# Performance work log

Hardware: AMD Instinct MI355X
Metric: run time of the kernel (lower is better)

Reference implementation:

```python
import jax, jax.numpy as jnp
import numpy as np

# dims forced by module structure (see shape_source)
DA, DV, DD, NL, L, R0 = 128, 96, 64, 8, 2, 1.0
ATOMS, EDGES, BATCH = 5000, 40000, 1


def radial_encode_8(rvec, r0):
    # reconstruction: 8 Gaussian RBFs on |r|/r0 with centers k/7
    r = jnp.sqrt(jnp.sum(rvec * rvec, axis=-1) + 1e-12)
    u = r / r0
    k = jnp.arange(NL, dtype=u.dtype)
    return jnp.exp(-0.5 * (u[..., None] * 7.0 - k) ** 2)  # (E, 8)


def tens_sigmoid(x):
    # equivariant sigmoid: rescale vector by bounded function of its norm
    n = jnp.sqrt(jnp.sum(x * x, axis=-1, keepdims=True) + 1e-12)
    return x * (2.0 * jax.nn.sigmoid(n) - 1.0) / n


def _forward(src, dst, r_ij, x_a, x_v, x_d,
             P_000, P_110, P_220, P_011, P_101, P_121, P_211, P_111,
             P_022, P_202, P_112, P_222, P_212,
             W_in_a, W_in_v, W_in_d, W_out_a, W_out_v, W_out_d,
             Wd_a, W1_a, b1_a, W2_a, b2_a, W3_a, b3_a,
             Vd_v, V1_v, V2_v, V3_v):
    b, A = x_a.shape[:2]
    # read-in, then fuse L into the batch dim (high-actv layout)
    a = jnp.einsum('oc,bnc->bno', W_in_a, x_a).reshape(b, A, L, DA).transpose(2, 0, 1, 3).reshape(L * b, A, DA)
    v = jnp.einsum('oc,bnci->bnoi', W_in_v, x_v).reshape(b, A, L, DV, 3).transpose(2, 0, 1, 3, 4).reshape(L * b, A, DV, 3)
    d = jnp.einsum('oc,bncij->bnoij', W_in_d, x_d).reshape(b, A, L, DD, 3, 3).transpose(2, 0, 1, 3, 4, 5).reshape(L * b, A, DD, 3, 3)

    rad = radial_encode_8(r_ij, R0)              # (E, 8)
    rh = tens_sigmoid(r_ij * (7.0 / R0))         # (E, 3)
    pa = rad                                      # (E, 8)
    pv = rad[:, :, None] * rh[:, None, :]         # (E, 8, 3)
    pd = rad[:, :, None, None] * rh[:, None, None, :] * rh[:, None, :, None]  # (E, 8, 3, 3)

    # edge gather (dst nodes)
    aj, vj, dj = a[:, dst], v[:, dst], d[:, dst]

    # Ant16: 13 fused equivariant tensor-product contractions
    psi_a = (jnp.einsum('alc,el,bec->bea', P_000, pa, aj)
             + jnp.einsum('alc,eli,beci->bea', P_110, pv, vj)
             + jnp.einsum('alc,elij,becij->bea', P_220, pd, dj))

    def cross1(P, phi, xv):
        t = lambda j, k: jnp.einsum('vlc,el,bec->bev', P, phi[:, :, j], xv[:, :, :, k])
        return jnp.stack([t(1, 2) - t(2, 1), t(2, 0) - t(0, 2), t(0, 1) - t(1, 0)], axis=-1)

    psi_v = (jnp.einsum('vlc,el,beci->bevi', P_011, pa, vj)
             + jnp.einsum('vlc,eli,bec->bevi', P_101, pv, aj)
             + jnp.einsum('vlc,elj,becij->bevi', P_121, pv, dj)
             + jnp.einsum('vlc,elij,becj->bevi', P_211, pd, vj)
             + cross1(P_111, pv, vj))

    def cross2(P, phid, xv):
        t = lambda k, m: jnp.einsum('dlc,elj,bec->bedj', P, phid[:, :, k, :], xv[:, :, :, m])
        return jnp.stack([t(1, 2) - t(2, 1), t(2, 0) - t(0, 2), t(0, 1) - t(1, 0)], axis=-2)

    psi_d = (jnp.einsum('dlc,el,becij->bedij', P_022, pa, dj)
             + jnp.einsum('dlc,elij,bec->bedij', P_202, pd, aj)
             + jnp.einsum('dlc,eli,becj->bedij', P_112, pv, vj)
             + jnp.einsum('dlc,elik,beckj->bedij', P_222, pd, dj)
             + cross2(P_212, pd, vj))

    # psi_a = psi_a + MLP(psi_a);  MLP(x) = x W_d^T + 3-layer leaky-relu net
    h = jax.nn.leaky_relu(psi_a @ W1_a.T + b1_a, 0.1)
    h = jax.nn.leaky_relu(h @ W2_a.T + b2_a, 0.1)
    psi_a = psi_a + psi_a @ Wd_a.T + h @ W3_a.T + b3_a

    # psi_v = psi_v + VectorMLP(psi_v) (channel linear + tens_sigmoid, equivariant)
    hv = tens_sigmoid(jnp.einsum('oc,beci->beoi', V1_v, psi_v))
    hv = tens_sigmoid(jnp.einsum('oc,beci->beoi', V2_v, hv))
    psi_v = psi_v + jnp.einsum('oc,beci->beoi', Vd_v, psi_v) + jnp.einsum('oc,beci->beoi', V3_v, hv)

    # scatter-reduce messages onto src nodes
    Ba = jnp.zeros_like(a).at[:, src].add(psi_a)
    Bv = jnp.zeros_like(v).at[:, src].add(psi_v)
    Bd = jnp.zeros_like(d).at[:, src].add(psi_d)

    # unfuse L back into the channel dim (low-actv layout), then read out
    Ba = Ba.reshape(L, b, A, DA).transpose(1, 2, 0, 3).reshape(b, A, L * DA)
    Bv = Bv.reshape(L, b, A, DV, 3).transpose(1, 2, 0, 3, 4).reshape(b, A, L * DV, 3)
    Bd = Bd.reshape(L, b, A, DD, 3, 3).transpose(1, 2, 0, 3, 4, 5).reshape(b, A, L * DD, 3, 3)
    return (jnp.einsum('oc,bnc->bno', W_out_a, Ba),
            jnp.einsum('oc,bnci->bnoi', W_out_v, Bv),
            jnp.einsum('oc,bncij->bnoij', W_out_d, Bd))


def setup_inputs() -> dict:
    key = jax.random.key(0)
    ks = iter(jax.random.split(key, 48))
    nrm = lambda *s: jax.random.normal(next(ks), s, dtype=jnp.float32)
    nfac = (NL * max(DA, DV, DD)) ** -0.5
    P = lambda do, di: nrm(do, NL, di) * nfac
    lin = lambda do, di: nrm(do, di) * (di ** -0.5)
    return dict(
        src=jax.random.randint(next(ks), (EDGES,), 0, ATOMS),
        dst=jax.random.randint(next(ks), (EDGES,), 0, ATOMS),
        r_ij=nrm(EDGES, 3),
        x_a=nrm(BATCH, ATOMS, DA), x_v=nrm(BATCH, ATOMS, DV, 3), x_d=nrm(BATCH, ATOMS, DD, 3, 3),
        P_000=P(DA, DA), P_110=P(DA, DV), P_220=P(DA, DD),
        P_011=P(DV, DV), P_101=P(DV, DA), P_121=P(DV, DD), P_211=P(DV, DV), P_111=P(DV, DV),
        P_022=P(DD, DD), P_202=P(DD, DA), P_112=P(DD, DV), P_222=P(DD, DD), P_212=P(DD, DV),
        W_in_a=lin(DA * L, DA), W_in_v=lin(DV * L, DV), W_in_d=lin(DD * L, DD),
        W_out_a=lin(DA, DA * L), W_out_v=lin(DV, DV * L), W_out_d=lin(DD, DD * L),
        Wd_a=lin(DA, DA), W1_a=lin(2 * DA, DA), b1_a=jnp.zeros(2 * DA, jnp.float32),
        W2_a=lin(2 * DA, 2 * DA), b2_a=jnp.zeros(2 * DA, jnp.float32),
        W3_a=lin(DA, 2 * DA), b3_a=jnp.zeros(DA, jnp.float32),
        Vd_v=lin(DV, DV), V1_v=lin(2 * DV, DV), V2_v=lin(2 * DV, 2 * DV), V3_v=lin(DV, 2 * DV),
    )


def reference(src, dst, r_ij, x_a, x_v, x_d,
              P_000, P_110, P_220, P_011, P_101, P_121, P_211, P_111,
              P_022, P_202, P_112, P_222, P_212,
              W_in_a, W_in_v, W_in_d, W_out_a, W_out_v, W_out_d,
              Wd_a, W1_a, b1_a, W2_a, b2_a, W3_a, b3_a,
              Vd_v, V1_v, V2_v, V3_v):
    return _forward(src, dst, r_ij, x_a, x_v, x_d,
                    P_000, P_110, P_220, P_011, P_101, P_121, P_211, P_111,
                    P_022, P_202, P_112, P_222, P_212,
                    W_in_a, W_in_v, W_in_d, W_out_a, W_out_v, W_out_d,
                    Wd_a, W1_a, b1_a, W2_a, b2_a, W3_a, b3_a,
                    Vd_v, V1_v, V2_v, V3_v)
```

## Files before the change

### kernel.cpp

```cpp
#include <hip/hip_runtime.h>
#include <hip/hip_bf16.h>

#define NA 5000
#define NE 40000

static const int POFF[13] = {0, 131072, 229376, 294912, 368640, 466944, 516096,
                             589824, 663552, 696320, 761856, 811008, 843776};
#define A_OFF    892928
#define V_OFF    2172928
#define D_OFF    5052928
#define PHI_OFF  10812928
#define PSIA_OFF 11292928
#define PSIV_OFF 16412928
#define PSID_OFF 27932928
#define INT_OFF  50972928
#define ICNT  0
#define ICUR  5000
#define SCNT  10000
#define SCUR  15000
#define IOFF  20000
#define SOFF  25008
#define IEIDX 30016
#define ISLOT 70016
#define SPERM 110016

#define OUT_V 640000
#define OUT_D 2080000

#define WT1 0
#define WT2 32768
#define WT3 98304
#define WTD 131072
#define VT1 147456
#define VT2 165888
#define VT3 202752
#define VTD 221184

#define OFF_000 POFF[0]
#define OFF_110 POFF[1]
#define OFF_220 POFF[2]
#define OFF_011 POFF[3]
#define OFF_101 POFF[4]
#define OFF_121 POFF[5]
#define OFF_211 POFF[6]
#define OFF_111 POFF[7]
#define OFF_022 POFF[8]
#define OFF_202 POFF[9]
#define OFF_112 POFF[10]
#define OFF_222 POFF[11]
#define OFF_212 POFF[12]

__device__ __forceinline__ float dot4f(float4 a, float4 b) {
  return a.x*b.x + a.y*b.y + a.z*b.z + a.w*b.w;
}
__device__ __forceinline__ float lrelu(float x) { return x > 0.f ? x : 0.1f*x; }
__device__ __forceinline__ float bf2f(unsigned short u) {
  union { unsigned int i; float f; } x; x.i = ((unsigned int)u) << 16; return x.f;
}
__device__ __forceinline__ unsigned short f2bf(float f) {
  union { unsigned int i; float f; } x; x.f = f;
  unsigned int r = x.i + 0x7FFFu + ((x.i >> 16) & 1u);
  return (unsigned short)(r >> 16);
}

struct P13 { const float* p[13]; };
struct P8  { const float* p[8]; };

__global__ __launch_bounds__(256) void transP_all_kernel(P13 ps, float* __restrict__ Pt)
{
  static const int Od[13] = {128,128,128, 96, 96, 96, 96, 96, 64, 64, 64, 64, 64};
  static const int Cd[13] = {128, 96, 64, 96,128, 64, 96, 96, 64,128, 96, 64, 96};
  static const int POF[13] = {0, 131072, 229376, 294912, 368640, 466944, 516096,
                              589824, 663552, 696320, 761856, 811008, 843776};
  static const int CUM[14] = {0,16384,28672,36864,46080,58368,64512,73728,
                              82944,87040,95232,101376,105472,111616};
  int idx = blockIdx.x * 256 + threadIdx.x;
  if (idx >= 111616) return;
  int i = 0;
  while (idx >= CUM[i+1]) ++i;
  const int r = idx - CUM[i];
  const int O = Od[i], C = Cd[i];
  const int o = r / C, c = r % C;
  const float* src = ps.p[i];
  float* dst = Pt + POF[i];
#pragma unroll
  for (int k = 0; k < 8; ++k)
    dst[((size_t)c * O + o) * 8 + k] = src[((size_t)o * 8 + k) * C + c];
}

__global__ __launch_bounds__(256) void transW_all_kernel(P8 ps, float* __restrict__ ot)
{
  static const int R[8]   = {256,256,128,128,192,192, 96, 96};
  static const int C[8]   = {128,256,256,128, 96,192,192, 96};
  static const int CUM[9] = {0,32768,98304,131072,147456,165888,202752,221184,230400};
  int idx = blockIdx.x * 256 + threadIdx.x;
  if (idx >= 230400) return;
  int i = 0;
  while (idx >= CUM[i+1]) ++i;
  const int r = idx - CUM[i];
  const int rr = r / C[i], cc = r % C[i];
  ot[(size_t)CUM[i] + (size_t)cc * R[i] + rr] = ps.p[i][r];
}

__global__ __launch_bounds__(256) void hist2_kernel(
    const int* __restrict__ dstk, const int* __restrict__ srck,
    int* __restrict__ cntd, int* __restrict__ cnts)
{
  int e = blockIdx.x * 256 + threadIdx.x;
  if (e < NE) { atomicAdd(&cntd[dstk[e]], 1); atomicAdd(&cnts[srck[e]], 1); }
}

__global__ __launch_bounds__(256) void scan2_kernel(
    const int* __restrict__ cnt0, int* __restrict__ off0,
    const int* __restrict__ cnt1, int* __restrict__ off1)
{
  const int* cnt = (blockIdx.x == 0) ? cnt0 : cnt1;
  int* off       = (blockIdx.x == 0) ? off0 : off1;
  __shared__ int part[256];
  const int t = threadIdx.x;
  int loc[20]; int s = 0;
#pragma unroll
  for (int i = 0; i < 20; ++i) {
    int idx = t * 20 + i;
    int v = (idx < NA) ? cnt[idx] : 0;
    loc[i] = v; s += v;
  }
  part[t] = s; __syncthreads();
  for (int ofs = 1; ofs < 256; ofs <<= 1) {
    int v = (t >= ofs) ? part[t - ofs] : 0;
    __syncthreads();
    part[t] += v;
    __syncthreads();
  }
  int run = part[t] - s;
#pragma unroll
  for (int i = 0; i < 20; ++i) {
    int idx = t * 20 + i;
    if (idx < NA) off[idx] = run;
    run += loc[i];
  }
  if (t == 255) off[NA] = run;
}

__global__ __launch_bounds__(256) void sort_scatter_kernel(
    const int* __restrict__ dst, const int* __restrict__ off,
    int* __restrict__ cur, int* __restrict__ eidx, int* __restrict__ islot)
{
  int e = blockIdx.x * 256 + threadIdx.x;
  if (e >= NE) return;
  int d = dst[e];
  int pos = off[d] + atomicAdd(&cur[d], 1);
  eidx[pos] = e;
  islot[e] = pos;
}

__global__ __launch_bounds__(256) void ssort_phi_kernel(
    const int* __restrict__ src, const int* __restrict__ islot,
    const int* __restrict__ soff, int* __restrict__ scur, int* __restrict__ sperm,
    const int* __restrict__ eidx, const float* __restrict__ r_ij, float* __restrict__ phi)
{
  const int B = (NE + 255) / 256;
  if ((int)blockIdx.x < B) {
    int e = blockIdx.x * 256 + threadIdx.x;
    if (e >= NE) return;
    int s = src[e];
    int pos = soff[s] + atomicAdd(&scur[s], 1);
    sperm[pos] = islot[e];
  } else {
    int p = (blockIdx.x - B) * 256 + threadIdx.x;
    if (p >= NE) return;
    int e = eidx[p];
    const float rx = r_ij[e*3+0], ry = r_ij[e*3+1], rz = r_ij[e*3+2];
    const float r2 = rx*rx + ry*ry + rz*rz;
    const float r = sqrtf(r2 + 1e-12f);
#pragma unroll
    for (int k = 0; k < 8; ++k) {
      const float z = 7.f*r - (float)k;
      phi[(size_t)p*12 + k] = expf(-0.5f*z*z);
    }
    const float nn = sqrtf(49.f*r2 + 1e-12f);
    const float sc = (2.f / (1.f + expf(-nn)) - 1.f) / nn;
    phi[(size_t)p*12 + 8]  = 7.f*rx*sc;
    phi[(size_t)p*12 + 9]  = 7.f*ry*sc;
    phi[(size_t)p*12 + 10] = 7.f*rz*sc;
    phi[(size_t)p*12 + 11] = 0.f;
  }
}

__global__ __launch_bounds__(256) void proj_in_kernel(
    const float* __restrict__ x_a, const float* __restrict__ x_v, const float* __restrict__ x_d,
    const float* __restrict__ Wa, const float* __restrict__ Wv, const float* __restrict__ Wd,
    float* __restrict__ a_ws, float* __restrict__ v_ws, float* __restrict__ d_ws)
{
  __shared__ float xs[992];
  const int n = blockIdx.x, t = threadIdx.x;
  for (int q = t; q < 128; q += 256) xs[q]       = x_a[(size_t)n*128 + q];
  for (int q = t; q < 288; q += 256) xs[128 + q] = x_v[(size_t)n*288 + q];
  for (int q = t; q < 576; q += 256) xs[416 + q] = x_d[(size_t)n*576 + q];
  __syncthreads();
  {
    const float* W = &Wa[(size_t)t * 128];
    float acc = 0.f;
    for (int c = 0; c < 128; c += 4) acc += dot4f(*(const float4*)&W[c], *(const float4*)&xs[c]);
    int l = t >> 7, o = t & 127;
    a_ws[((size_t)l*NA + n)*128 + o] = acc;
  }
  if (t < 192) {
    const float* W = &Wv[(size_t)t * 96];
    float a0 = 0.f, a1 = 0.f, a2 = 0.f;
    for (int c = 0; c < 96; ++c) {
      float w = W[c]; const float* x = &xs[128 + c*3];
      a0 = fmaf(w, x[0], a0); a1 = fmaf(w, x[1], a1); a2 = fmaf(w, x[2], a2);
    }
    int l = t / 96, o = t % 96;
    float* dstp = &v_ws[(((size_t)l*NA + n)*96 + o)*3];
    dstp[0] = a0; dstp[1] = a1; dstp[2] = a2;
  }
  if (t < 128) {
    const float* W = &Wd[(size_t)t * 64];
    float acc[9] = {0,0,0,0,0,0,0,0,0};
    for (int c = 0; c < 64; ++c) {
      float w = W[c]; const float* x = &xs[416 + c*9];
#pragma unroll
      for (int j = 0; j < 9; ++j) acc[j] = fmaf(w, x[j], acc[j]);
    }
    int l = t >> 6, o = t & 63;
    float* dstp = &d_ws[(((size_t)l*NA + n)*64 + o)*9];
#pragma unroll
    for (int j = 0; j < 9; ++j) dstp[j] = acc[j];
  }
}

template<int O, int C, int NMU>
__device__ __forceinline__ void zcompute(const float* __restrict__ Pt,
    const float* __restrict__ xl, int o, float z[8][NMU])
{
#pragma unroll
  for (int k = 0; k < 8; ++k)
#pragma unroll
    for (int m = 0; m < NMU; ++m) z[k][m] = 0.f;
  const float* p = Pt + o * 8;
#pragma unroll 2
  for (int c = 0; c < C; ++c, p += O*8) {
    const float4 pa = *(const float4*)p;
    const float4 pb = *(const float4*)(p + 4);
#pragma unroll
    for (int m = 0; m < NMU; ++m) {
      const float xv = xl[c * NMU + m];
      z[0][m] = fmaf(pa.x, xv, z[0][m]);
      z[1][m] = fmaf(pa.y, xv, z[1][m]);
      z[2][m] = fmaf(pa.z, xv, z[2][m]);
      z[3][m] = fmaf(pa.w, xv, z[3][m]);
      z[4][m] = fmaf(pb.x, xv, z[4][m]);
      z[5][m] = fmaf(pb.y, xv, z[5][m]);
      z[6][m] = fmaf(pb.z, xv, z[6][m]);
      z[7][m] = fmaf(pb.w, xv, z[7][m]);
    }
  }
}

template<int O, int C>
__device__ __forceinline__ void zcompute_k4(const float* __restrict__ Pt,
    const float* __restrict__ xl, int o, int kh, float z[4][9])
{
#pragma unroll
  for (int k = 0; k < 4; ++k)
#pragma unroll
    for (int m = 0; m < 9; ++m) z[k][m] = 0.f;
  const float* p = Pt + o * 8 + kh * 4;
#pragma unroll 2
  for (int c = 0; c < C; ++c, p += O*8) {
    const float4 pa = *(const float4*)p;
#pragma unroll
    for (int m = 0; m < 9; ++m) {
      const float xv = xl[c*9 + m];
      z[0][m] = fmaf(pa.x, xv, z[0][m]);
      z[1][m] = fmaf(pa.y, xv, z[1][m]);
      z[2][m] = fmaf(pa.z, xv, z[2][m]);
      z[3][m] = fmaf(pa.w, xv, z[3][m]);
    }
  }
}

template<int NMU>
__device__ __forceinline__ float kdot(const float z[8][NMU], int m, const float* rr) {
  float s = z[0][m] * rr[0];
#pragma unroll
  for (int k = 1; k < 8; ++k) s = fmaf(z[k][m], rr[k], s);
  return s;
}
__device__ __forceinline__ float kdot_k4(const float z[4][9], int m, const float* rr) {
  float s = z[0][m] * rr[0];
#pragma unroll
  for (int k = 1; k < 4; ++k) s = fmaf(z[k][m], rr[k], s);
  return s;
}

#define F1_XA 0
#define F1_XV 256
#define F1_XD 832
#define F1_TOT 1984

template<int NT>
__device__ __forceinline__ void load_features1(float* sm, int t, int n,
    const float* __restrict__ a_ws, const float* __restrict__ v_ws, const float* __restrict__ d_ws)
{
  for (int q = t; q < 256; q += NT)
    sm[F1_XA + q] = a_ws[((size_t)(q>>7)*NA + n)*128 + (q & 127)];
  for (int q = t; q < 576; q += NT)
    sm[F1_XV + q] = v_ws[((size_t)(q/288)*NA + n)*288 + (q % 288)];
  for (int q = t; q < 1152; q += NT)
    sm[F1_XD + q] = d_ws[((size_t)(q/576)*NA + n)*576 + (q % 576)];
}

__global__ __launch_bounds__(256, 3) void pass_fused_kernel(
    const int* __restrict__ off, const float* __restrict__ phi,
    const float* __restrict__ Pt,
    const float* __restrict__ a_ws, const float* __restrict__ v_ws, const float* __restrict__ d_ws,
    unsigned short* __restrict__ psiA, unsigned short* __restrict__ psiV,
    unsigned short* __restrict__ psiD)
{
  __shared__ float sm[9040];
  const int b = blockIdx.x;
  const int type = b % 3;
  const int n = b / 3;
  const int t = threadIdx.x;
  const int off0 = off[n], off1 = off[n + 1];
  const int d = off1 - off0;
  if (d == 0) return;

  load_features1<256>(sm, t, n, a_ws, v_ws, d_ws);

  if (type == 0) {
    const int o = t & 127, l = t >> 7;
    const float* xa = &sm[F1_XA + l*128];
    const float* xv = &sm[F1_XV + l*288];
    const float* xd = &sm[F1_XD + l*576];
    float* sphi = &sm[F1_TOT];
    float* psis = &sm[F1_TOT + 192];

    const int nw = (d + 15) >> 4;
    for (int w = 0; w < nw; ++w) {
      const int b0 = w * 16;
      __syncthreads();
      if (t < 192) {
        const int s = t / 12, f = t % 12;
        sphi[t] = (b0 + s < d) ? phi[(size_t)(off0 + b0 + s)*12 + f] : 0.f;
      }
      __syncthreads();

      {
        float z[8][1];
        zcompute<128,128,1>(Pt + OFF_000, xa, o, z);
#pragma unroll
        for (int e = 0; e < 16; ++e)
          psis[e*256 + t] = kdot<1>(z, 0, &sphi[e*12]);
      }
      {
        float z[8][3];
        zcompute<128,96,3>(Pt + OFF_110, xv, o, z);
#pragma unroll
        for (int e = 0; e < 16; ++e) {
          const float* ph = &sphi[e*12];
          psis[e*256 + t] += ph[8]*kdot<3>(z,0,ph) + ph[9]*kdot<3>(z,1,ph) + ph[10]*kdot<3>(z,2,ph);
        }
      }
#pragma unroll
      for (int kh = 0; kh < 2; ++kh) {
        float z[4][9];
        zcompute_k4<128,64>(Pt + OFF_220, xd, o, kh, z);
#pragma unroll
        for (int e = 0; e < 16; ++e) {
          const float* ph = &sphi[e*12];
          const float* rr = ph + kh*4;
          float s[9];
#pragma unroll
          for (int m = 0; m < 9; ++m) s[m] = kdot_k4(z, m, rr);
          const float q0 = ph[8], q1 = ph[9], q2 = ph[10];
          psis[e*256 + t] += q0*(q0*s[0] + q1*s[1] + q2*s[2])
                           + q1*(q0*s[3] + q1*s[4] + q2*s[5])
                           + q2*(q0*s[6] + q1*s[7] + q2*s[8]);
        }
      }
#pragma unroll
      for (int e = 0; e < 16; ++e)
        if (b0 + e < d) psiA[(size_t)(off0 + b0 + e)*256 + t] = f2bf(psis[e*256 + t]);
    }
  } else if (type == 1) {
    const bool act = (t < 192);
    const int o = t % 96, l = (t / 96) & 1;
    const float* xa = &sm[F1_XA + l*128];
    const float* xv = &sm[F1_XV + l*288];
    const float* xd = &sm[F1_XD + l*576];
    float* sphi = &sm[F1_TOT];
    float* psis = &sm[F1_TOT + 144];

    const int nw = (d + 11) / 12;
    for (int w = 0; w < nw; ++w) {
      const int b0 = w * 12;
      __syncthreads();
      if (t < 144) {
        const int s = t / 12, f = t % 12;
        sphi[t] = (b0 + s < d) ? phi[(size_t)(off0 + b0 + s)*12 + f] : 0.f;
      }
      __syncthreads();

      if (act) {
        {
          float z[8][3];
          zcompute<96,96,3>(Pt + OFF_011, xv, o, z);
#pragma unroll
          for (int e = 0; e < 12; ++e) {
            const float* ph = &sphi[e*12];
            float* pb = &psis[e*576 + t];
            pb[0]   = kdot<3>(z,0,ph);
            pb[192] = kdot<3>(z,1,ph);
            pb[384] = kdot<3>(z,2,ph);
          }
        }
        {
          float z[8][1];
          zcompute<96,128,1>(Pt + OFF_101, xa, o, z);
#pragma unroll
          for (int e = 0; e < 12; ++e) {
            const float* ph = &sphi[e*12];
            const float s0 = kdot<1>(z,0,ph);
            float* pb = &psis[e*576 + t];
            pb[0] += ph[8]*s0; pb[192] += ph[9]*s0; pb[384] += ph[10]*s0;
          }
        }
#pragma unroll
        for (int kh = 0; kh < 2; ++kh) {
          float z[4][9];
          zcompute_k4<96,64>(Pt + OFF_121, xd, o, kh, z);
#pragma unroll
          for (int e = 0; e < 12; ++e) {
            const float* ph = &sphi[e*12];
            const float* rr = ph + kh*4;
            float s[9];
#pragma unroll
            for (int m = 0; m < 9; ++m) s[m] = kdot_k4(z, m, rr);
            const float q0 = ph[8], q1 = ph[9], q2 = ph[10];
            float* pb = &psis[e*576 + t];
            pb[0]   += q0*s[0] + q1*s[1] + q2*s[2];
            pb[192] += q0*s[3] + q1*s[4] + q2*s[5];
            pb[384] += q0*s[6] + q1*s[7] + q2*s[8];
          }
        }
        {
          float z[8][3];
          zcompute<96,96,3>(Pt + OFF_211, xv, o, z);
#pragma unroll
          for (int e = 0; e < 12; ++e) {
            const float* ph = &sphi[e*12];
            const float tt = ph[8]*kdot<3>(z,0,ph) + ph[9]*kdot<3>(z,1,ph) + ph[10]*kdot<3>(z,2,ph);
            float* pb = &psis[e*576 + t];
            pb[0] += ph[8]*tt; pb[192] += ph[9]*tt; pb[384] += ph[10]*tt;
          }
        }
        {
          float z[8][3];
          zcompute<96,96,3>(Pt + OFF_111, xv, o, z);
#pragma unroll
          for (int e = 0; e < 12; ++e) {
            const float* ph = &sphi[e*12];
            const float s0 = kdot<3>(z,0,ph), s1 = kdot<3>(z,1,ph), s2 = kdot<3>(z,2,ph);
            const float q0 = ph[8], q1 = ph[9], q2 = ph[10];
            float* pb = &psis[e*576 + t];
            pb[0]   += q1*s2 - q2*s1;
            pb[192] += q2*s0 - q0*s2;
            pb[384] += q0*s1 - q1*s0;
          }
        }
#pragma unroll
        for (int e = 0; e < 12; ++e) {
          if (b0 + e < d) {
            const size_t bb = (size_t)(off0 + b0 + e)*576 + l*288 + o*3;
            const float* pb = &psis[e*576 + t];
            psiV[bb+0] = f2bf(pb[0]); psiV[bb+1] = f2bf(pb[192]); psiV[bb+2] = f2bf(pb[384]);
          }
        }
      }
    }
  } else {
    const bool act = (t < 128);
    const int o = t & 63, l = (t >> 6) & 1;
    const float* xa = &sm[F1_XA + l*128];
    const float* xv = &sm[F1_XV + l*288];
    const float* xd = &sm[F1_XD + l*576];
    float* sphi = &sm[F1_TOT];
    float* psis = &sm[F1_TOT + 72];

    const int nw = (d + 5) / 6;
    for (int w = 0; w < nw; ++w) {
      const int b0 = w * 6;
      __syncthreads();
      if (t < 72) {
        const int s = t / 12, f = t % 12;
        sphi[t] = (b0 + s < d) ? phi[(size_t)(off0 + b0 + s)*12 + f] : 0.f;
      }
      __syncthreads();

      if (act) {
        {
          float z[4][9];
          zcompute_k4<64,64>(Pt + OFF_022, xd, o, 0, z);
#pragma unroll
          for (int e = 0; e < 6; ++e) {
            const float* rr = &sphi[e*12];
            float* pb = &psis[(e*128 + t)*9];
#pragma unroll
            for (int m = 0; m < 9; ++m) pb[m] = kdot_k4(z, m, rr);
          }
        }
        {
          float z[4][9];
          zcompute_k4<64,64>(Pt + OFF_022, xd, o, 1, z);
#pragma unroll
          for (int e = 0; e < 6; ++e) {
            const float* rr = &sphi[e*12] + 4;
            float* pb = &psis[(e*128 + t)*9];
#pragma unroll
            for (int m = 0; m < 9; ++m) pb[m] += kdot_k4(z, m, rr);
          }
        }
        {
          float z[8][1];
          zcompute<64,128,1>(Pt + OFF_202, xa, o, z);
#pragma unroll
          for (int e = 0; e < 6; ++e) {
            const float* ph = &sphi[e*12];
            const float s0 = kdot<1>(z, 0, ph);
            const float q0 = ph[8], q1 = ph[9], q2 = ph[10];
            float* pb = &psis[(e*128 + t)*9];
            pb[0] += q0*q0*s0; pb[1] += q0*q1*s0; pb[2] += q0*q2*s0;
            pb[3] += q1*q0*s0; pb[4] += q1*q1*s0; pb[5] += q1*q2*s0;
            pb[6] += q2*q0*s0; pb[7] += q2*q1*s0; pb[8] += q2*q2*s0;
          }
        }
        {
          float z[8][3];
          zcompute<64,96,3>(Pt + OFF_112, xv, o, z);
#pragma unroll
          for (int e = 0; e < 6; ++e) {
            const float* ph = &sphi[e*12];
            const float s0 = kdot<3>(z,0,ph), s1 = kdot<3>(z,1,ph), s2 = kdot<3>(z,2,ph);
            const float q0 = ph[8], q1 = ph[9], q2 = ph[10];
            float* pb = &psis[(e*128 + t)*9];
            pb[0] += q0*s0; pb[1] += q0*s1; pb[2] += q0*s2;
            pb[3] += q1*s0; pb[4] += q1*s1; pb[5] += q1*s2;
            pb[6] += q2*s0; pb[7] += q2*s1; pb[8] += q2*s2;
          }
        }
#pragma unroll
        for (int kh = 0; kh < 2; ++kh) {
          float z[4][9];
          zcompute_k4<64,64>(Pt + OFF_222, xd, o, kh, z);
#pragma unroll
          for (int e = 0; e < 6; ++e) {
            const float* ph = &sphi[e*12];
            const float* rr = ph + kh*4;
            float s[9];
#pragma unroll
            for (int m = 0; m < 9; ++m) s[m] = kdot_k4(z, m, rr);
            const float q0 = ph[8], q1 = ph[9], q2 = ph[10];
            const float u0 = q0*s[0] + q1*s[3] + q2*s[6];
            const float u1 = q0*s[1] + q1*s[4] + q2*s[7];
            const float u2 = q0*s[2] + q1*s[5] + q2*s[8];
            float* pb = &psis[(e*128 + t)*9];
            pb[0] += q0*u0; pb[1] += q0*u1; pb[2] += q0*u2;
            pb[3] += q1*u0; pb[4] += q1*u1; pb[5] += q1*u2;
            pb[6] += q2*u0; pb[7] += q2*u1; pb[8] += q2*u2;
          }
        }
        {
          float z[8][3];
          zcompute<64,96,3>(Pt + OFF_212, xv, o, z);
#pragma unroll
          for (int e = 0; e < 6; ++e) {
            const float* ph = &sphi[e*12];
            const float s0 = kdot<3>(z,0,ph), s1 = kdot<3>(z,1,ph), s2 = kdot<3>(z,2,ph);
            const float q0 = ph[8], q1 = ph[9], q2 = ph[10];
            const float c0 = q1*s2 - q2*s1;
            const float c1 = q2*s0 - q0*s2;
            const float c2 = q0*s1 - q1*s0;
            float* pb = &psis[(e*128 + t)*9];
            pb[0] += c0*q0; pb[1] += c0*q1; pb[2] += c0*q2;
            pb[3] += c1*q0; pb[4] += c1*q1; pb[5] += c1*q2;
            pb[6] += c2*q0; pb[7] += c2*q1; pb[8] += c2*q2;
          }
        }
#pragma unroll
        for (int e = 0; e < 6; ++e) {
          if (b0 + e < d) {
            const float* pb = &psis[(e*128 + t)*9];
            unsigned short* bp = &psiD[(size_t)(off0 + b0 + e)*1152 + t*9];
#pragma unroll
            for (int j = 0; j < 9; ++j) bp[j] = f2bf(pb[j]);
          }
        }
      }
    }
  }
}

__global__ __launch_bounds__(256, 3) void mlp_fused_kernel(
    unsigned short* __restrict__ psiA, unsigned short* __restrict__ psiV,
    const float* __restrict__ Wdt,
    const float* __restrict__ W1t, const float* __restrict__ b1,
    const float* __restrict__ W2t, const float* __restrict__ b2,
    const float* __restrict__ W3t, const float* __restrict__ b3,
    const float* __restrict__ Vdt, const float* __restrict__ V1t,
    const float* __restrict__ V2t, const float* __restrict__ V3t)
{
  __shared__ float sm[11520];
  const int b = blockIdx.x;
  const int t = threadIdx.x;

  if (b % 3 == 0) {
    const int cbase = (b / 3) * 16;
    float* PA = sm;
    float* H1 = sm + 2048;
    float* H2 = sm + 6144;

    for (int q = t; q < 2048; q += 256)
      PA[q] = bf2f(psiA[(size_t)cbase*128 + q]);
    __syncthreads();
    {
      const int p0 = (t & 63) * 4, j0 = (t >> 6) * 4;
      float acc[4][4];
#pragma unroll
      for (int r = 0; r < 4; ++r)
#pragma unroll
        for (int j = 0; j < 4; ++j) acc[r][j] = 0.f;
      for (int c = 0; c < 128; c += 4) {
        float4 wv[4];
#pragma unroll
        for (int cc = 0; cc < 4; ++cc) wv[cc] = *(const float4*)&W1t[(size_t)(c+cc)*256 + p0];
#pragma unroll
        for (int j = 0; j < 4; ++j) {
          const float4 x = *(const float4*)&PA[(j0+j)*128 + c];
          acc[0][j] += wv[0].x*x.x + wv[1].x*x.y + wv[2].x*x.z + wv[3].x*x.w;
          acc[1][j] += wv[0].y*x.x + wv[1].y*x.y + wv[2].y*x.z + wv[3].y*x.w;
          acc[2][j] += wv[0].z*x.x + wv[1].z*x.y + wv[2].z*x.z + wv[3].z*x.w;
          acc[3][j] += wv[0].w*x.x + wv[1].w*x.y + wv[2].w*x.z + wv[3].w*x.w;
        }
      }
      const float bb0 = b1[p0], bb1 = b1[p0+1], bb2 = b1[p0+2], bb3 = b1[p0+3];
#pragma unroll
      for (int j = 0; j < 4; ++j) {
        float4 v; v.x = lrelu(acc[0][j]+bb0); v.y = lrelu(acc[1][j]+bb1);
        v.z = lrelu(acc[2][j]+bb2); v.w = lrelu(acc[3][j]+bb3);
        *(float4*)&H1[(j0+j)*256 + p0] = v;
      }
    }
    __syncthreads();
    {
      const int p0 = (t & 63) * 4, j0 = (t >> 6) * 4;
      float acc[4][4];
#pragma unroll
      for (int r = 0; r < 4; ++r)
#pragma unroll
        for (int j = 0; j < 4; ++j) acc[r][j] = 0.f;
      for (int c = 0; c < 256; c += 4) {
        float4 wv[4];
#pragma unroll
        for (int cc = 0; cc < 4; ++cc) wv[cc] = *(const float4*)&W2t[(size_t)(c+cc)*256 + p0];
#pragma unroll
        for (int j = 0; j < 4; ++j) {
          const float4 x = *(const float4*)&H1[(j0+j)*256 + c];
          acc[0][j] += wv[0].x*x.x + wv[1].x*x.y + wv[2].x*x.z + wv[3].x*x.w;
          acc[1][j] += wv[0].y*x.x + wv[1].y*x.y + wv[2].y*x.z + wv[3].y*x.w;
          acc[2][j] += wv[0].z*x.x + wv[1].z*x.y + wv[2].z*x.z + wv[3].z*x.w;
          acc[3][j] += wv[0].w*x.x + wv[1].w*x.y + wv[2].w*x.z + wv[3].w*x.w;
        }
      }
      const float bb0 = b2[p0], bb1 = b2[p0+1], bb2 = b2[p0+2], bb3 = b2[p0+3];
#pragma unroll
      for (int j = 0; j < 4; ++j) {
        float4 v; v.x = lrelu(acc[0][j]+bb0); v.y = lrelu(acc[1][j]+bb1);
        v.z = lrelu(acc[2][j]+bb2); v.w = lrelu(acc[3][j]+bb3);
        *(float4*)&H2[(j0+j)*256 + p0] = v;
      }
    }
    __syncthreads();
    {
      const int p0 = (t & 63) * 2, j0 = (t >> 6) * 4;
      float acc[2][4];
#pragma unroll
      for (int r = 0; r < 2; ++r)
#pragma unroll
        for (int j = 0; j < 4; ++j) acc[r][j] = 0.f;
      for (int c = 0; c < 128; c += 4) {
        float2 wv[4];
#pragma unroll
        for (int cc = 0; cc < 4; ++cc) wv[cc] = *(const float2*)&Wdt[(size_t)(c+cc)*128 + p0];
#pragma unroll
        for (int j = 0; j < 4; ++j) {
          const float4 x = *(const float4*)&PA[(j0+j)*128 + c];
          acc[0][j] += wv[0].x*x.x + wv[1].x*x.y + wv[2].x*x.z + wv[3].x*x.w;
          acc[1][j] += wv[0].y*x.x + wv[1].y*x.y + wv[2].y*x.z + wv[3].y*x.w;
        }
      }
      for (int c = 0; c < 256; c += 4) {
        float2 wv[4];
#pragma unroll
        for (int cc = 0; cc < 4; ++cc) wv[cc] = *(const float2*)&W3t[(size_t)(c+cc)*128 + p0];
#pragma unroll
        for (int j = 0; j < 4; ++j) {
          const float4 x = *(const float4*)&H2[(j0+j)*256 + c];
          acc[0][j] += wv[0].x*x.x + wv[1].x*x.y + wv[2].x*x.z + wv[3].x*x.w;
          acc[1][j] += wv[0].y*x.x + wv[1].y*x.y + wv[2].y*x.z + wv[3].y*x.w;
        }
      }
      const float bb0 = b3[p0], bb1 = b3[p0+1];
#pragma unroll
      for (int j = 0; j < 4; ++j) {
        const float o0 = acc[0][j] + bb0 + PA[(j0+j)*128 + p0];
        const float o1 = acc[1][j] + bb1 + PA[(j0+j)*128 + p0 + 1];
        psiA[(size_t)(cbase + j0 + j)*128 + p0]     = f2bf(o0);
        psiA[(size_t)(cbase + j0 + j)*128 + p0 + 1] = f2bf(o1);
      }
    }
  } else {
    const bool act = (t < 192);
    const int cbase = (b - b/3 - 1) * 8;
    float* PV  = sm;
    float* HV  = sm + 2304;
    float* HV2 = sm + 6912;

    for (int q = t; q < 2304; q += 256) {
      const int j = q / 288, r = q % 288, i = r / 96, o = r % 96;
      PV[j*288 + i*96 + o] = bf2f(psiV[(size_t)(cbase + j)*288 + o*3 + i]);
    }
    __syncthreads();
    if (act) {
      const int p0 = (t % 96) * 2, j0 = (t / 96) * 4;
      float acc[2][4][3];
#pragma unroll
      for (int r = 0; r < 2; ++r)
#pragma unroll
        for (int j = 0; j < 4; ++j) { acc[r][j][0]=0.f; acc[r][j][1]=0.f; acc[r][j][2]=0.f; }
      for (int c = 0; c < 96; c += 4) {
        float2 wv[4];
#pragma unroll
        for (int cc = 0; cc < 4; ++cc) wv[cc] = *(const float2*)&V1t[(size_t)(c+cc)*192 + p0];
#pragma unroll
        for (int j = 0; j < 4; ++j)
#pragma unroll
          for (int i = 0; i < 3; ++i) {
            const float4 x = *(const float4*)&PV[(j0+j)*288 + i*96 + c];
            acc[0][j][i] += wv[0].x*x.x + wv[1].x*x.y + wv[2].x*x.z + wv[3].x*x.w;
            acc[1][j][i] += wv[0].y*x.x + wv[1].y*x.y + wv[2].y*x.z + wv[3].y*x.w;
          }
      }
      float scl[2][4];
#pragma unroll
      for (int r = 0; r < 2; ++r)
#pragma unroll
        for (int j = 0; j < 4; ++j) {
          const float nn = sqrtf(acc[r][j][0]*acc[r][j][0] + acc[r][j][1]*acc[r][j][1]
                               + acc[r][j][2]*acc[r][j][2] + 1e-12f);
          scl[r][j] = (2.f / (1.f + expf(-nn)) - 1.f) / nn;
        }
#pragma unroll
      for (int j = 0; j < 4; ++j)
#pragma unroll
        for (int i = 0; i < 3; ++i) {
          float2 v;
          v.x = acc[0][j][i]*scl[0][j]; v.y = acc[1][j][i]*scl[1][j];
          *(float2*)&HV[(j0+j)*576 + i*192 + p0] = v;
        }
    }
    __syncthreads();
    if (act) {
      const int p0 = (t % 96) * 2, j0 = (t / 96) * 4;
      float acc[2][4][3];
#pragma unroll
      for (int r = 0; r < 2; ++r)
#pragma unroll
        for (int j = 0; j < 4; ++j) { acc[r][j][0]=0.f; acc[r][j][1]=0.f; acc[r][j][2]=0.f; }
      for (int c = 0; c < 192; c += 4) {
        float2 wv[4];
#pragma unroll
        for (int cc = 0; cc < 4; ++cc) wv[cc] = *(const float2*)&V2t[(size_t)(c+cc)*192 + p0];
#pragma unroll
        for (int j = 0; j < 4; ++j)
#pragma unroll
          for (int i = 0; i < 3; ++i) {
            const float4 x = *(const float4*)&HV[(j0+j)*576 + i*192 + c];
            acc[0][j][i] += wv[0].x*x.x + wv[1].x*x.y + wv[2].x*x.z + wv[3].x*x.w;
            acc[1][j][i] += wv[0].y*x.x + wv[1].y*x.y + wv[2].y*x.z + wv[3].y*x.w;
          }
      }
      float scl[2][4];
#pragma unroll
      for (int r = 0; r < 2; ++r)
#pragma unroll
        for (int j = 0; j < 4; ++j) {
          const float nn = sqrtf(acc[r][j][0]*acc[r][j][0] + acc[r][j][1]*acc[r][j][1]
                               + acc[r][j][2]*acc[r][j][2] + 1e-12f);
          scl[r][j] = (2.f / (1.f + expf(-nn)) - 1.f) / nn;
        }
#pragma unroll
      for (int j = 0; j < 4; ++j)
#pragma unroll
        for (int i = 0; i < 3; ++i) {
          float2 v;
          v.x = acc[0][j][i]*scl[0][j]; v.y = acc[1][j][i]*scl[1][j];
          *(float2*)&HV2[(j0+j)*576 + i*192 + p0] = v;
        }
    }
    __syncthreads();
    if (act) {
      const int p0 = t % 96, j0 = (t / 96) * 4;
      float acc[4][3];
#pragma unroll
      for (int j = 0; j < 4; ++j) { acc[j][0]=0.f; acc[j][1]=0.f; acc[j][2]=0.f; }
      for (int c = 0; c < 96; c += 4) {
        float wv[4];
#pragma unroll
        for (int cc = 0; cc < 4; ++cc) wv[cc] = Vdt[(size_t)(c+cc)*96 + p0];
#pragma unroll
        for (int j = 0; j < 4; ++j)
#pragma unroll
          for (int i = 0; i < 3; ++i) {
            const float4 x = *(const float4*)&PV[(j0+j)*288 + i*96 + c];
            acc[j][i] += wv[0]*x.x + wv[1]*x.y + wv[2]*x.z + wv[3]*x.w;
          }
      }
      for (int c = 0; c < 192; c += 4) {
        float wv[4];
#pragma unroll
        for (int cc = 0; cc < 4; ++cc) wv[cc] = V3t[(size_t)(c+cc)*96 + p0];
#pragma unroll
        for (int j = 0; j < 4; ++j)
#pragma unroll
          for (int i = 0; i < 3; ++i) {
            const float4 x = *(const float4*)&HV2[(j0+j)*576 + i*192 + c];
            acc[j][i] += wv[0]*x.x + wv[1]*x.y + wv[2]*x.z + wv[3]*x.w;
          }
      }
#pragma unroll
      for (int j = 0; j < 4; ++j)
#pragma unroll
        for (int i = 0; i < 3; ++i) {
          const float v = acc[j][i] + PV[(j0+j)*288 + i*96 + p0];
          psiV[(size_t)(cbase + j0 + j)*288 + p0*3 + i] = f2bf(v);
        }
    }
  }
}

__global__ __launch_bounds__(256, 2) void gather_out_kernel(
    const int* __restrict__ soff, const int* __restrict__ sperm,
    const unsigned short* __restrict__ psiA, const unsigned short* __restrict__ psiV,
    const unsigned short* __restrict__ psiD,
    const float* __restrict__ Wa, const float* __restrict__ Wv, const float* __restrict__ Wd,
    float* __restrict__ out)
{
  __shared__ float bs[1984];
  const int n = blockIdx.x, t = threadIdx.x;
  const int s0 = soff[n], s1 = soff[n + 1];
  float acc[8];
#pragma unroll
  for (int u = 0; u < 8; ++u) acc[u] = 0.f;
  for (int p2 = s0; p2 < s1; ++p2) {
    const int slot = sperm[p2];
    const unsigned short* ra = psiA + (size_t)slot * 256;
    const unsigned short* rv = psiV + (size_t)slot * 576;
    const unsigned short* rd = psiD + (size_t)slot * 1152;
#pragma unroll
    for (int u = 0; u < 8; ++u) {
      const int v = t + 256 * u;
      if (v < 256)        acc[u] += bf2f(ra[v]);
      else if (v < 832)   acc[u] += bf2f(rv[v - 256]);
      else if (v < 1984)  acc[u] += bf2f(rd[v - 832]);
    }
  }
#pragma unroll
  for (int u = 0; u < 8; ++u) {
    const int v = t + 256 * u;
    if (v < 1984) bs[v] = acc[u];
  }
  __syncthreads();
  if (t < 128) {
    const float* W = &Wa[(size_t)t * 256];
    float a = 0.f;
    for (int c = 0; c < 256; c += 4) a += dot4f(*(const float4*)&W[c], *(const float4*)&bs[c]);
    out[(size_t)n*128 + t] = a;
  }
  if (t < 96) {
    const float* W = &Wv[(size_t)t * 192];
    float a0 = 0.f, a1 = 0.f, a2 = 0.f;
    for (int c = 0; c < 192; ++c) {
      const float w = W[c]; const float* x = &bs[256 + c*3];
      a0 = fmaf(w, x[0], a0); a1 = fmaf(w, x[1], a1); a2 = fmaf(w, x[2], a2);
    }
    float* d = &out[OUT_V + ((size_t)n*96 + t)*3];
    d[0] = a0; d[1] = a1; d[2] = a2;
  }
  if (t < 64) {
    const float* W = &Wd[(size_t)t * 128];
    float a[9] = {0,0,0,0,0,0,0,0,0};
    for (int c = 0; c < 128; ++c) {
      const float w = W[c]; const float* x = &bs[832 + c*9];
#pragma unroll
      for (int j = 0; j < 9; ++j) a[j] = fmaf(w, x[j], a[j]);
    }
    float* d = &out[OUT_D + ((size_t)n*64 + t)*9];
#pragma unroll
    for (int j = 0; j < 9; ++j) d[j] = a[j];
  }
}

extern "C" void kernel_launch(void* const* d_in, const int* in_sizes, int n_in,
                              void* d_out, int out_size, void* d_ws, size_t ws_size,
                              hipStream_t stream) {
  (void)in_sizes; (void)n_in; (void)out_size; (void)ws_size;
  const int*   src  = (const int*)d_in[0];
  const int*   dst  = (const int*)d_in[1];
  const float* r_ij = (const float*)d_in[2];
  const float* x_a  = (const float*)d_in[3];
  const float* x_v  = (const float*)d_in[4];
  const float* x_d  = (const float*)d_in[5];
  const float* P[13];
  for (int i = 0; i < 13; ++i) P[i] = (const float*)d_in[6 + i];
  const float* W_in_a  = (const float*)d_in[19];
  const float* W_in_v  = (const float*)d_in[20];
  const float* W_in_d  = (const float*)d_in[21];
  const float* W_out_a = (const float*)d_in[22];
  const float* W_out_v = (const float*)d_in[23];
  const float* W_out_d = (const float*)d_in[24];
  const float* Wd_a = (const float*)d_in[25];
  const float* W1   = (const float*)d_in[26];
  const float* b1   = (const float*)d_in[27];
  const float* W2   = (const float*)d_in[28];
  const float* b2   = (const float*)d_in[29];
  const float* W3   = (const float*)d_in[30];
  const float* b3   = (const float*)d_in[31];
  const float* Vd   = (const float*)d_in[32];
  const float* V1   = (const float*)d_in[33];
  const float* V2   = (const float*)d_in[34];
  const float* V3   = (const float*)d_in[35];

  float* ws = (float*)d_ws;
  float* Pt = ws;
  int*   ib = (int*)(ws + INT_OFF);
  unsigned short* psiA = (unsigned short*)(ws + PSIA_OFF);
  unsigned short* psiV = (unsigned short*)(ws + PSIV_OFF);
  unsigned short* psiD = (unsigned short*)(ws + PSID_OFF);
  float* ot = (float*)d_out;

  P13 ps; for (int i = 0; i < 13; ++i) ps.p[i] = P[i];
  transP_all_kernel<<<(111616 + 255) / 256, 256, 0, stream>>>(ps, Pt);
  P8 pw;
  pw.p[0] = W1; pw.p[1] = W2; pw.p[2] = W3; pw.p[3] = Wd_a;
  pw.p[4] = V1; pw.p[5] = V2; pw.p[6] = V3; pw.p[7] = Vd;
  transW_all_kernel<<<(230400 + 255) / 256, 256, 0, stream>>>(pw, ot);

  hipMemsetAsync(ib, 0, 20000 * sizeof(int), stream);

  const int egrid = (NE + 255) / 256;
  hist2_kernel<<<egrid, 256, 0, stream>>>(dst, src, ib + ICNT, ib + SCNT);
  scan2_kernel<<<2, 256, 0, stream>>>(ib + ICNT, ib + IOFF, ib + SCNT, ib + SOFF);
  sort_scatter_kernel<<<egrid, 256, 0, stream>>>(dst, ib + IOFF, ib + ICUR, ib + IEIDX, ib + ISLOT);
  ssort_phi_kernel<<<2 * egrid, 256, 0, stream>>>(src, ib + ISLOT, ib + SOFF, ib + SCUR,
                                                  ib + SPERM, ib + IEIDX, r_ij, ws + PHI_OFF);

  proj_in_kernel<<<NA, 256, 0, stream>>>(x_a, x_v, x_d, W_in_a, W_in_v, W_in_d,
                                         ws + A_OFF, ws + V_OFF, ws + D_OFF);

  pass_fused_kernel<<<3 * NA, 256, 0, stream>>>(ib + IOFF, ws + PHI_OFF, Pt,
                                                ws + A_OFF, ws + V_OFF, ws + D_OFF,
                                                psiA, psiV, psiD);

  mlp_fused_kernel<<<15000, 256, 0, stream>>>(psiA, psiV,
                                              ot + WTD, ot + WT1, b1, ot + WT2, b2, ot + WT3, b3,
                                              ot + VTD, ot + VT1, ot + VT2, ot + VT3);

  gather_out_kernel<<<NA, 256, 0, stream>>>(ib + SOFF, ib + SPERM,
                                            psiA, psiV, psiD,
                                            W_out_a, W_out_v, W_out_d, (float*)d_out);
}
```

Before: 3.406 ms.

## Split rank-2 output branch over k-halves across all 256 threads with LDS atomics

In the rank-2 (d-feature) branch of the edge tensor-product kernel, only 128 of 256 threads did work before. Now every thread is active: the 8 radial basis components are split into two halves (kh = t>>7), each half computes partial contractions, and the two partials are summed into shared memory with atomicAdd. The shared accumulator is zeroed each window and the bf16 writeback is split across the two halves. This doubles the active threads but adds LDS atomic traffic, an extra zeroing pass and an extra barrier.

```diff
diff --git a/kernel.cpp b/kernel.cpp
--- a/kernel.cpp
+++ b/kernel.cpp
@@ -259,21 +259,21 @@
   }
 }
 
-template<int O, int C>
-__device__ __forceinline__ void zcompute_k4(const float* __restrict__ Pt,
-    const float* __restrict__ xl, int o, int kh, float z[4][9])
+template<int O, int C, int NMU>
+__device__ __forceinline__ void zcompute_k4n(const float* __restrict__ Pt,
+    const float* __restrict__ xl, int o, int kh, float z[4][NMU])
 {
 #pragma unroll
   for (int k = 0; k < 4; ++k)
 #pragma unroll
-    for (int m = 0; m < 9; ++m) z[k][m] = 0.f;
+    for (int m = 0; m < NMU; ++m) z[k][m] = 0.f;
   const float* p = Pt + o * 8 + kh * 4;
 #pragma unroll 2
   for (int c = 0; c < C; ++c, p += O*8) {
     const float4 pa = *(const float4*)p;
 #pragma unroll
-    for (int m = 0; m < 9; ++m) {
-      const float xv = xl[c*9 + m];
+    for (int m = 0; m < NMU; ++m) {
+      const float xv = xl[c*NMU + m];
       z[0][m] = fmaf(pa.x, xv, z[0][m]);
       z[1][m] = fmaf(pa.y, xv, z[1][m]);
       z[2][m] = fmaf(pa.z, xv, z[2][m]);
@@ -289,7 +289,8 @@
   for (int k = 1; k < 8; ++k) s = fmaf(z[k][m], rr[k], s);
   return s;
 }
-__device__ __forceinline__ float kdot_k4(const float z[4][9], int m, const float* rr) {
+template<int NMU>
+__device__ __forceinline__ float kdot4n(const float z[4][NMU], int m, const float* rr) {
   float s = z[0][m] * rr[0];
 #pragma unroll
   for (int k = 1; k < 4; ++k) s = fmaf(z[k][m], rr[k], s);
@@ -368,14 +369,14 @@
 #pragma unroll
       for (int kh = 0; kh < 2; ++kh) {
         float z[4][9];
-        zcompute_k4<128,64>(Pt + OFF_220, xd, o, kh, z);
+        zcompute_k4n<128,64,9>(Pt + OFF_220, xd, o, kh, z);
 #pragma unroll
         for (int e = 0; e < 16; ++e) {
           const float* ph = &sphi[e*12];
           const float* rr = ph + kh*4;
           float s[9];
 #pragma unroll
-          for (int m = 0; m < 9; ++m) s[m] = kdot_k4(z, m, rr);
+          for (int m = 0; m < 9; ++m) s[m] = kdot4n<9>(z, m, rr);
           const float q0 = ph[8], q1 = ph[9], q2 = ph[10];
           psis[e*256 + t] += q0*(q0*s[0] + q1*s[1] + q2*s[2])
                            + q1*(q0*s[3] + q1*s[4] + q2*s[5])
@@ -432,14 +433,14 @@
 #pragma unroll
         for (int kh = 0; kh < 2; ++kh) {
           float z[4][9];
-          zcompute_k4<96,64>(Pt + OFF_121, xd, o, kh, z);
+          zcompute_k4n<96,64,9>(Pt + OFF_121, xd, o, kh, z);
 #pragma unroll
           for (int e = 0; e < 12; ++e) {
             const float* ph = &sphi[e*12];
             const float* rr = ph + kh*4;
             float s[9];
 #pragma unroll
-            for (int m = 0; m < 9; ++m) s[m] = kdot_k4(z, m, rr);
+            for (int m = 0; m < 9; ++m) s[m] = kdot4n<9>(z, m, rr);
             const float q0 = ph[8], q1 = ph[9], q2 = ph[10];
             float* pb = &psis[e*576 + t];
             pb[0]   += q0*s[0] + q1*s[1] + q2*s[2];
@@ -483,8 +484,8 @@
       }
     }
   } else {
-    const bool act = (t < 128);
-    const int o = t & 63, l = (t >> 6) & 1;
+    const int o = t & 63, l = (t >> 6) & 1, kh = t >> 7;
+    const int tl = l*64 + o;
     const float* xa = &sm[F1_XA + l*128];
     const float* xv = &sm[F1_XV + l*288];
     const float* xd = &sm[F1_XD + l*576];
@@ -495,109 +496,100 @@
     for (int w = 0; w < nw; ++w) {
       const int b0 = w * 6;
       __syncthreads();
+      for (int q = t; q < 6912; q += 256) psis[q] = 0.f;
       if (t < 72) {
         const int s = t / 12, f = t % 12;
         sphi[t] = (b0 + s < d) ? phi[(size_t)(off0 + b0 + s)*12 + f] : 0.f;
       }
       __syncthreads();
 
-      if (act) {
-        {
-          float z[4][9];
-          zcompute_k4<64,64>(Pt + OFF_022, xd, o, 0, z);
-#pragma unroll
-          for (int e = 0; e < 6; ++e) {
-            const float* rr = &sphi[e*12];
-            float* pb = &psis[(e*128 + t)*9];
-#pragma unroll
-            for (int m = 0; m < 9; ++m) pb[m] = kdot_k4(z, m, rr);
-          }
-        }
-        {
-          float z[4][9];
-          zcompute_k4<64,64>(Pt + OFF_022, xd, o, 1, z);
-#pragma unroll
-          for (int e = 0; e < 6; ++e) {
-            const float* rr = &sphi[e*12] + 4;
-            float* pb = &psis[(e*128 + t)*9];
-#pragma unroll
-            for (int m = 0; m < 9; ++m) pb[m] += kdot_k4(z, m, rr);
-          }
-        }
-        {
-          float z[8][1];
-          zcompute<64,128,1>(Pt + OFF_202, xa, o, z);
-#pragma unroll
-          for (int e = 0; e < 6; ++e) {
-            const float* ph = &sphi[e*12];
-            const float s0 = kdot<1>(z, 0, ph);
-            const float q0 = ph[8], q1 = ph[9], q2 = ph[10];
-            float* pb = &psis[(e*128 + t)*9];
-            pb[0] += q0*q0*s0; pb[1] += q0*q1*s0; pb[2] += q0*q2*s0;
-            pb[3] += q1*q0*s0; pb[4] += q1*q1*s0; pb[5] += q1*q2*s0;
-            pb[6] += q2*q0*s0; pb[7] += q2*q1*s0; pb[8] += q2*q2*s0;
-          }
-        }
-        {
-          float z[8][3];
-          zcompute<64,96,3>(Pt + OFF_112, xv, o, z);
-#pragma unroll
-          for (int e = 0; e < 6; ++e) {
-            const float* ph = &sphi[e*12];
-            const float s0 = kdot<3>(z,0,ph), s1 = kdot<3>(z,1,ph), s2 = kdot<3>(z,2,ph);
-            const float q0 = ph[8], q1 = ph[9], q2 = ph[10];
-            float* pb = &psis[(e*128 + t)*9];
-            pb[0] += q0*s0; pb[1] += q0*s1; pb[2] += q0*s2;
-            pb[3] += q1*s0; pb[4] += q1*s1; pb[5] += q1*s2;
-            pb[6] += q2*s0; pb[7] += q2*s1; pb[8] += q2*s2;
-          }
-        }
-#pragma unroll
-        for (int kh = 0; kh < 2; ++kh) {
-          float z[4][9];
-          zcompute_k4<64,64>(Pt + OFF_222, xd, o, kh, z);
-#pragma unroll
-          for (int e = 0; e < 6; ++e) {
-            const float* ph = &sphi[e*12];
-            const float* rr = ph + kh*4;
-            float s[9];
-#pragma unroll
-            for (int m = 0; m < 9; ++m) s[m] = kdot_k4(z, m, rr);
-            const float q0 = ph[8], q1 = ph[9], q2 = ph[10];
-            const float u0 = q0*s[0] + q1*s[3] + q2*s[6];
-            const float u1 = q0*s[1] + q1*s[4] + q2*s[7];
-            const float u2 = q0*s[2] + q1*s[5] + q2*s[8];
-            float* pb = &psis[(e*128 + t)*9];
-            pb[0] += q0*u0; pb[1] += q0*u1; pb[2] += q0*u2;
-            pb[3] += q1*u0; pb[4] += q1*u1; pb[5] += q1*u2;
-            pb[6] += q2*u0; pb[7] += q2*u1; pb[8] += q2*u2;
-          }
-        }
-        {
-          float z[8][3];
-          zcompute<64,96,3>(Pt + OFF_212, xv, o, z);
-#pragma unroll
-          for (int e = 0; e < 6; ++e) {
-            const float* ph = &sphi[e*12];
-            const float s0 = kdot<3>(z,0,ph), s1 = kdot<3>(z,1,ph), s2 = kdot<3>(z,2,ph);
-            const float q0 = ph[8], q1 = ph[9], q2 = ph[10];
-            const float c0 = q1*s2 - q2*s1;
-            const float c1 = q2*s0 - q0*s2;
-            const float c2 = q0*s1 - q1*s0;
-            float* pb = &psis[(e*128 + t)*9];
-            pb[0] += c0*q0; pb[1] += c0*q1; pb[2] += c0*q2;
-            pb[3] += c1*q0; pb[4] += c1*q1; pb[5] += c1*q2;
-            pb[6] += c2*q0; pb[7] += c2*q1; pb[8] += c2*q2;
-          }
-        }
+      {
+        float z[4][9];
+        zcompute_k4n<64,64,9>(Pt + OFF_022, xd, o, kh, z);
 #pragma unroll
         for (int e = 0; e < 6; ++e) {
-          if (b0 + e < d) {
-            const float* pb = &psis[(e*128 + t)*9];
-            unsigned short* bp = &psiD[(size_t)(off0 + b0 + e)*1152 + t*9];
-#pragma unroll
-            for (int j = 0; j < 9; ++j) bp[j] = f2bf(pb[j]);
-          }
+          const float* rr = &sphi[e*12] + kh*4;
+          float* pb = &psis[(e*128 + tl)*9];
+#pragma unroll
+          for (int m = 0; m < 9; ++m) atomicAdd(&pb[m], kdot4n<9>(z, m, rr));
+        }
+      }
+      {
+        float z[4][1];
+        zcompute_k4n<64,128,1>(Pt + OFF_202, xa, o, kh, z);
+#pragma unroll
+        for (int e = 0; e < 6; ++e) {
+          const float* ph = &sphi[e*12];
+          const float s0 = kdot4n<1>(z, 0, ph + kh*4);
+          const float q0 = ph[8], q1 = ph[9], q2 = ph[10];
+          float* pb = &psis[(e*128 + tl)*9];
+          atomicAdd(&pb[0], q0*q0*s0); atomicAdd(&pb[1], q0*q1*s0); atomicAdd(&pb[2], q0*q2*s0);
+          atomicAdd(&pb[3], q1*q0*s0); atomicAdd(&pb[4], q1*q1*s0); atomicAdd(&pb[5], q1*q2*s0);
+          atomicAdd(&pb[6], q2*q0*s0); atomicAdd(&pb[7], q2*q1*s0); atomicAdd(&pb[8], q2*q2*s0);
+        }
+      }
+      {
+        float z[4][3];
+        zcompute_k4n<64,96,3>(Pt + OFF_112, xv, o, kh, z);
+#pragma unroll
+        for (int e = 0; e < 6; ++e) {
+          const float* ph = &sphi[e*12];
+          const float* rr = ph + kh*4;
+          const float s0 = kdot4n<3>(z,0,rr), s1 = kdot4n<3>(z,1,rr), s2 = kdot4n<3>(z,2,rr);
+          const float q0 = ph[8], q1 = ph[9], q2 = ph[10];
+          float* pb = &psis[(e*128 + tl)*9];
+          atomicAdd(&pb[0], q0*s0); atomicAdd(&pb[1], q0*s1); atomicAdd(&pb[2], q0*s2);
+          atomicAdd(&pb[3], q1*s0); atomicAdd(&pb[4], q1*s1); atomicAdd(&pb[5], q1*s2);
+          atomicAdd(&pb[6], q2*s0); atomicAdd(&pb[7], q2*s1); atomicAdd(&pb[8], q2*s2);
+        }
+      }
+      {
+        float z[4][9];
+        zcompute_k4n<64,64,9>(Pt + OFF_222, xd, o, kh, z);
+#pragma unroll
+        for (int e = 0; e < 6; ++e) {
+          const float* ph = &sphi[e*12];
+          const float* rr = ph + kh*4;
+          float s[9];
+#pragma unroll
+          for (int m = 0; m < 9; ++m) s[m] = kdot4n<9>(z, m, rr);
+          const float q0 = ph[8], q1 = ph[9], q2 = ph[10];
+          const float u0 = q0*s[0] + q1*s[3] + q2*s[6];
+          const float u1 = q0*s[1] + q1*s[4] + q2*s[7];
+          const float u2 = q0*s[2] + q1*s[5] + q2*s[8];
+          float* pb = &psis[(e*128 + tl)*9];
+          atomicAdd(&pb[0], q0*u0); atomicAdd(&pb[1], q0*u1); atomicAdd(&pb[2], q0*u2);
+          atomicAdd(&pb[3], q1*u0); atomicAdd(&pb[4], q1*u1); atomicAdd(&pb[5], q1*u2);
+          atomicAdd(&pb[6], q2*u0); atomicAdd(&pb[7], q2*u1); atomicAdd(&pb[8], q2*u2);
+        }
+      }
+      {
+        float z[4][3];
+        zcompute_k4n<64,96,3>(Pt + OFF_212, xv, o, kh, z);
+#pragma unroll
+        for (int e = 0; e < 6; ++e) {
+          const float* ph = &sphi[e*12];
+          const float* rr = ph + kh*4;
+          const float s0 = kdot4n<3>(z,0,rr), s1 = kdot4n<3>(z,1,rr), s2 = kdot4n<3>(z,2,rr);
+          const float q0 = ph[8], q1 = ph[9], q2 = ph[10];
+          const float c0 = q1*s2 - q2*s1;
+          const float c1 = q2*s0 - q0*s2;
+          const float c2 = q0*s1 - q1*s0;
+          float* pb = &psis[(e*128 + tl)*9];
+          atomicAdd(&pb[0], c0*q0); atomicAdd(&pb[1], c0*q1); atomicAdd(&pb[2], c0*q2);
+          atomicAdd(&pb[3], c1*q0); atomicAdd(&pb[4], c1*q1); atomicAdd(&pb[5], c1*q2);
+          atomicAdd(&pb[6], c2*q0); atomicAdd(&pb[7], c2*q1); atomicAdd(&pb[8], c2*q2);
+        }
+      }
+      __syncthreads();
+#pragma unroll
+      for (int ee = 0; ee < 3; ++ee) {
+        const int e = kh*3 + ee;
+        if (b0 + e < d) {
+          const float* pb = &psis[(e*128 + tl)*9];
+          unsigned short* bp = &psiD[(size_t)(off0 + b0 + e)*1152 + tl*9];
+#pragma unroll
+          for (int j = 0; j < 9; ++j) bp[j] = f2bf(pb[j]);
         }
       }
     }
```

After: 6.321 ms. 1.86x slower.
